# Performance work log

Measured on AMD Instinct MI355X. Metric: run time of the kernel, lower is better.

Reference implementation:

```python
import jax, jax.numpy as jnp
import numpy as np

B, S, L, D, M = 32, 256, 64, 100, 20  # batch, n_sentences, max_sentence_len, embed_dim, n_memories


def setup_inputs() -> dict:
    key = jax.random.key(0)
    ks = jax.random.split(key, 6)
    batch = jax.random.normal(ks[0], (B, S, L, D), dtype=jnp.float32)
    enc_mult = jnp.ones((L, D), dtype=jnp.float32)  # input_encoder_multiplier (init to ones)
    keys = 0.1 * jax.random.normal(ks[1], (M, D), dtype=jnp.float32)
    U = 0.1 * jax.random.normal(ks[2], (D, D), dtype=jnp.float32)  # nn.Linear weight [out,in]
    V = 0.1 * jax.random.normal(ks[3], (D, D), dtype=jnp.float32)
    W = 0.1 * jax.random.normal(ks[4], (D, D), dtype=jnp.float32)
    prelu_a = jnp.ones((), dtype=jnp.float32)  # PReLU(init=1), single shared parameter
    return {"batch": batch, "enc_mult": enc_mult, "keys": keys, "U": U, "V": V, "W": W, "prelu_a": prelu_a}


def reference(batch, enc_mult, keys, U, V, W, prelu_a):
    # Encode: elementwise multiply by learned positional multiplier, sum over words -> [B, S, D]
    enc = (batch * enc_mult).sum(axis=2)

    def prelu(x):
        return jnp.where(x >= 0, x, prelu_a * x)

    # keys @ V.T is step-invariant
    keysV = jnp.einsum('md,ed->me', keys, V)  # [M, D]

    def step(mem, s):  # mem: [B, M, D], s: [B, D]
        memory_gate = jnp.einsum('bd,bmd->bm', s, mem)          # [B, M]
        key_gate = jnp.einsum('bd,md->bm', s, keys)              # [B, M]
        gate = jax.nn.sigmoid(memory_gate + key_gate)            # [B, M]
        cand = prelu(
            jnp.einsum('bmd,ed->bme', mem, U)                    # U(memories)
            + keysV[None, :, :]                                  # V(keys)
            + jnp.einsum('bd,ed->be', s, W)[:, None, :]          # W(sentence), broadcast over M
        )
        mem = mem + cand * gate[:, :, None]
        mem = mem / jnp.linalg.norm(mem, axis=2, keepdims=True)  # L2 normalize each memory slot
        return mem, None

    mem0 = jnp.broadcast_to(keys[None, :, :], (B, M, D))  # memories init = keys repeated per batch
    mem_final, _ = jax.lax.scan(step, mem0, jnp.swapaxes(enc, 0, 1))  # scan over sentences
    return mem_final
```

## Files before the change

### kernel.cpp

```cpp
#include <hip/hip_runtime.h>


typedef float v2f __attribute__((ext_vector_type(2)));

__global__ __launch_bounds__(256) void encode_k(
    const float* __restrict__ batch,
    const float* __restrict__ encm,
    float* __restrict__ enc)
{
    const int tid = blockIdx.x * 256 + threadIdx.x;
    const int r = tid / 25;
    const int c = tid % 25;
    const float4* b4 = (const float4*)batch + (size_t)r * 1600 + c;
    const float4* e4 = (const float4*)encm + c;
    float4 a0 = {0.f,0.f,0.f,0.f}, a1 = {0.f,0.f,0.f,0.f};
    #pragma unroll 8
    for (int l = 0; l < 64; l += 2) {
        float4 x0 = b4[l * 25],       mu0 = e4[l * 25];
        float4 x1 = b4[(l + 1) * 25], mu1 = e4[(l + 1) * 25];
        a0.x += x0.x * mu0.x; a0.y += x0.y * mu0.y; a0.z += x0.z * mu0.z; a0.w += x0.w * mu0.w;
        a1.x += x1.x * mu1.x; a1.y += x1.y * mu1.y; a1.z += x1.z * mu1.z; a1.w += x1.w * mu1.w;
    }
    float4 s;
    s.x = a0.x + a1.x; s.y = a0.y + a1.y; s.z = a0.z + a1.z; s.w = a0.w + a1.w;
    ((float4*)enc)[(size_t)r * 25 + c] = s;
}

__global__ void prep_k(const float* __restrict__ W,
                       const float* __restrict__ keys,
                       float* __restrict__ T)
{
    const int d = blockIdx.x;
    const int e = threadIdx.x;
    float v = 0.f;
    if (e < 100) v = W[e * 100 + d];
    else if (e < 120) v = keys[(e - 100) * 100 + d];
    T[d * 128 + e] = v;
}

__global__ __launch_bounds__(128) void project_k(
    const float* __restrict__ enc,
    const float* __restrict__ T,
    float* __restrict__ sWp,
    float* __restrict__ kg)
{
    __shared__ float encS[400];
    const int t = threadIdx.x;
    const int row0 = blockIdx.x * 4;
    if (t < 100) ((float4*)encS)[t] = ((const float4*)(enc + (size_t)row0 * 100))[t];
    __syncthreads();
    float a0 = 0.f, a1 = 0.f, a2 = 0.f, a3 = 0.f;
    #pragma unroll 4
    for (int d = 0; d < 100; ++d) {
        const float w = T[d * 128 + t];
        a0 += w * encS[d];
        a1 += w * encS[100 + d];
        a2 += w * encS[200 + d];
        a3 += w * encS[300 + d];
    }
    if (t < 100) {
        sWp[(size_t)row0 * 100 + t]       = a0;
        sWp[(size_t)(row0 + 1) * 100 + t] = a1;
        sWp[(size_t)(row0 + 2) * 100 + t] = a2;
        sWp[(size_t)(row0 + 3) * 100 + t] = a3;
    } else if (t < 120) {
        const int m = t - 100;
        kg[(size_t)row0 * 20 + m]       = a0;
        kg[(size_t)(row0 + 1) * 20 + m] = a1;
        kg[(size_t)(row0 + 2) * 20 + m] = a2;
        kg[(size_t)(row0 + 3) * 20 + m] = a3;
    }
}

template <int CTRL>
__device__ __forceinline__ float dpp_add_f(float x) {
    int s = __builtin_amdgcn_update_dpp(0, __float_as_int(x), CTRL, 0xF, 0xF, true);
    return x + __int_as_float(s);
}
__device__ __forceinline__ float lane63(float x) {
    return __int_as_float(__builtin_amdgcn_readlane(__float_as_int(x), 63));
}

#define MATVEC100(RES, SRC4)                                                   \
    {                                                                          \
        v2f A0 = {0.f,0.f}, A1 = {0.f,0.f}, A2 = {0.f,0.f}, A3 = {0.f,0.f};    \
        _Pragma("unroll")                                                      \
        for (int k = 0; k < 25; ++k) {                                         \
            float4 v = (SRC4)[k];                                              \
            A0 += Upk[4 * k + 0] * v.x;                                        \
            A1 += Upk[4 * k + 1] * v.y;                                        \
            A2 += Upk[4 * k + 2] * v.z;                                        \
            A3 += Upk[4 * k + 3] * v.w;                                        \
        }                                                                      \
        RES = (A0 + A1) + (A2 + A3);                                           \
    }

__global__ __launch_bounds__(64, 1) void entnet_scan(
    const float* __restrict__ enc,
    const float* __restrict__ sWp,
    const float* __restrict__ kg,
    const float* __restrict__ keys,
    const float* __restrict__ U,
    const float* __restrict__ V,
    const float* __restrict__ paPtr,
    float* __restrict__ out)
{
    __shared__ float4 cand4[32];
    float* candF = (float*)cand4;
    const int lane = threadIdx.x;
    const int b = blockIdx.x / 20;
    const int m = blockIdx.x % 20;
    const bool hi = (lane < 36);
    const float h = hi ? 1.f : 0.f;
    const int e0 = lane;
    const int e1 = hi ? (64 + lane) : 99;
    const float pa = paPtr[0];

    v2f Upk[100];
    {
        const float4* u0 = (const float4*)(U + e0 * 100);
        const float4* u1 = (const float4*)(U + e1 * 100);
        #pragma unroll
        for (int k = 0; k < 25; ++k) {
            float4 a = u0[k], c = u1[k];
            Upk[4 * k + 0] = (v2f){a.x, c.x};
            Upk[4 * k + 1] = (v2f){a.y, c.y};
            Upk[4 * k + 2] = (v2f){a.z, c.z};
            Upk[4 * k + 3] = (v2f){a.w, c.w};
        }
    }
    float kv0 = 0.f, kv1 = 0.f;
    {
        const float4* km = (const float4*)(keys + m * 100);
        const float4* v0 = (const float4*)(V + e0 * 100);
        const float4* v1 = (const float4*)(V + e1 * 100);
        #pragma unroll
        for (int k = 0; k < 25; ++k) {
            float4 kk = km[k], a = v0[k], c = v1[k];
            kv0 += a.x * kk.x + a.y * kk.y + a.z * kk.z + a.w * kk.w;
            kv1 += c.x * kk.x + c.y * kk.y + c.z * kk.z + c.w * kk.w;
        }
    }
    const float k0 = keys[m * 100 + e0];
    const float k1 = h * keys[m * 100 + e1];
    float nm0 = k0, nm1 = k1;
    candF[lane] = nm0;
    candF[64 + lane] = nm1;
    __asm__ __volatile__("" ::: "memory");

    v2f P;
    MATVEC100(P, cand4);

    float nq = k0 * k0 + k1 * k1;
    nq = dpp_add_f<0x111>(nq); nq = dpp_add_f<0x112>(nq); nq = dpp_add_f<0x114>(nq);
    nq = dpp_add_f<0x118>(nq); nq = dpp_add_f<0x142>(nq); nq = dpp_add_f<0x143>(nq);
    float nsq = lane63(nq);
    float rn = 1.f;

    const float* encRow = enc + (size_t)b * 25600;
    const float* sWRow  = sWp + (size_t)b * 25600;
    const float* kgRow  = kg + (size_t)b * 5120 + m;

    float sv0 = encRow[e0], sv1 = encRow[e1];
    float sw0 = sWRow[e0],  sw1 = sWRow[e1];
    float kgc = kgRow[0];

    for (int step = 0; step < 256; ++step) {
        const int nxt = (step < 255 ? step + 1 : 255);
        const float nsv0 = encRow[nxt * 100 + e0], nsv1 = encRow[nxt * 100 + e1];
        const float nsw0 = sWRow[nxt * 100 + e0], nsw1 = sWRow[nxt * 100 + e1];
        const float nkg  = kgRow[nxt * 20];

        const float x0 = rn * P.x + kv0 + sw0;
        const float x1 = rn * P.y + kv1 + sw1;
        float c0 = (x0 >= 0.f) ? x0 : pa * x0;
        float c1 = (x1 >= 0.f) ? x1 : pa * x1;
        c1 *= h;

        candF[lane] = c0;
        candF[64 + lane] = c1;
        __asm__ __volatile__("" ::: "memory");

        float q1 = sv0 * nm0 + sv1 * nm1;
        float q3 = nm0 * c0 + nm1 * c1;
        float p4 = c0 * c0 + c1 * c1;
        #define RND3(C) q1 = dpp_add_f<C>(q1); q3 = dpp_add_f<C>(q3); p4 = dpp_add_f<C>(p4);
        RND3(0x111) RND3(0x112) RND3(0x114) RND3(0x118) RND3(0x142) RND3(0x143)
        #undef RND3

        v2f Q;
        MATVEC100(Q, cand4);

        const float Q1 = lane63(q1);
        const float Q3 = lane63(q3);
        const float P4 = lane63(p4);

        const float g = 1.f / (1.f + __expf(-(rn * Q1 + kgc)));

        nm0 = rn * nm0 + g * c0;
        nm1 = rn * nm1 + g * c1;
        P = rn * P + g * Q;

        const float n2 = nsq + 2.f * (g * rn) * Q3 + g * g * P4;
        rn = rsqrtf(n2);
        nsq = 1.f;

        sv0 = nsv0; sv1 = nsv1; sw0 = nsw0; sw1 = nsw1; kgc = nkg;
    }
    float* orow = out + (size_t)(b * 20 + m) * 100;
    orow[e0] = nm0 * rn;
    if (hi) orow[e1] = nm1 * rn;
}

extern "C" void kernel_launch(void* const* d_in, const int* in_sizes, int n_in,
                              void* d_out, int out_size, void* d_ws, size_t ws_size,
                              hipStream_t stream) {
    const float* batch = (const float*)d_in[0];
    const float* encm  = (const float*)d_in[1];
    const float* keys  = (const float*)d_in[2];
    const float* U     = (const float*)d_in[3];
    const float* V     = (const float*)d_in[4];
    const float* W     = (const float*)d_in[5];
    const float* pa    = (const float*)d_in[6];
    float* out = (float*)d_out;

    float* enc = (float*)d_ws;
    float* sWp = enc + 819200;
    float* kgb = sWp + 819200;
    float* T   = kgb + 163840;

    encode_k<<<800, 256, 0, stream>>>(batch, encm, enc);
    prep_k<<<100, 128, 0, stream>>>(W, keys, T);
    project_k<<<2048, 128, 0, stream>>>(enc, T, sWp, kgb);
    entnet_scan<<<640, 64, 0, stream>>>(enc, sWp, kgb, keys, U, V, pa, out);
}
```

Before: 529.5 us.

## Restructure encode reduction via LDS and software-pipeline gate computation in scan

```diff
diff --git a/kernel.cpp b/kernel.cpp
--- a/kernel.cpp
+++ b/kernel.cpp
@@ -3,27 +3,41 @@
 
 typedef float v2f __attribute__((ext_vector_type(2)));
 
-__global__ __launch_bounds__(256) void encode_k(
+__global__ __launch_bounds__(320) void encode_k(
     const float* __restrict__ batch,
     const float* __restrict__ encm,
     float* __restrict__ enc)
 {
-    const int tid = blockIdx.x * 256 + threadIdx.x;
-    const int r = tid / 25;
-    const int c = tid % 25;
-    const float4* b4 = (const float4*)batch + (size_t)r * 1600 + c;
-    const float4* e4 = (const float4*)encm + c;
-    float4 a0 = {0.f,0.f,0.f,0.f}, a1 = {0.f,0.f,0.f,0.f};
-    #pragma unroll 8
-    for (int l = 0; l < 64; l += 2) {
-        float4 x0 = b4[l * 25],       mu0 = e4[l * 25];
-        float4 x1 = b4[(l + 1) * 25], mu1 = e4[(l + 1) * 25];
-        a0.x += x0.x * mu0.x; a0.y += x0.y * mu0.y; a0.z += x0.z * mu0.z; a0.w += x0.w * mu0.w;
-        a1.x += x1.x * mu1.x; a1.y += x1.y * mu1.y; a1.z += x1.z * mu1.z; a1.w += x1.w * mu1.w;
-    }
-    float4 s;
-    s.x = a0.x + a1.x; s.y = a0.y + a1.y; s.z = a0.z + a1.z; s.w = a0.w + a1.w;
-    ((float4*)enc)[(size_t)r * 25 + c] = s;
+    __shared__ float prod[6400];
+    __shared__ float part[200];
+    const int t = threadIdx.x;
+    const int row = blockIdx.x;
+    const float4* rb = (const float4*)batch + (size_t)row * 1600;
+    const float4* e4 = (const float4*)encm;
+    float4* p4 = (float4*)prod;
+    #pragma unroll
+    for (int i = 0; i < 5; ++i) {
+        const int idx = i * 320 + t;
+        float4 x = rb[idx];
+        float4 mu = e4[idx];
+        float4 p;
+        p.x = x.x * mu.x; p.y = x.y * mu.y; p.z = x.z * mu.z; p.w = x.w * mu.w;
+        p4[idx] = p;
+    }
+    __syncthreads();
+    if (t < 200) {
+        const int c = (t < 100) ? t : (t - 100);
+        const int l0 = (t < 100) ? 0 : 32;
+        float s0 = 0.f, s1 = 0.f;
+        #pragma unroll
+        for (int l = 0; l < 32; l += 2) {
+            s0 += prod[(l0 + l) * 100 + c];
+            s1 += prod[(l0 + l + 1) * 100 + c];
+        }
+        part[t] = s0 + s1;
+    }
+    __syncthreads();
+    if (t < 100) enc[(size_t)row * 100 + t] = part[t] + part[100 + t];
 }
 
 __global__ void prep_k(const float* __restrict__ W,
@@ -80,6 +94,8 @@
 __device__ __forceinline__ float lane63(float x) {
     return __int_as_float(__builtin_amdgcn_readlane(__float_as_int(x), 63));
 }
+#define DPP6(v) v = dpp_add_f<0x111>(v); v = dpp_add_f<0x112>(v); v = dpp_add_f<0x114>(v); \
+                v = dpp_add_f<0x118>(v); v = dpp_add_f<0x142>(v); v = dpp_add_f<0x143>(v);
 
 #define MATVEC100(RES, SRC4)                                                   \
     {                                                                          \
@@ -95,7 +111,8 @@
         RES = (A0 + A1) + (A2 + A3);                                           \
     }
 
-__global__ __launch_bounds__(64, 1) void entnet_scan(
+__global__ __attribute__((amdgpu_waves_per_eu(1, 1))) __launch_bounds__(64)
+void entnet_scan(
     const float* __restrict__ enc,
     const float* __restrict__ sWp,
     const float* __restrict__ kg,
@@ -152,8 +169,7 @@
     MATVEC100(P, cand4);
 
     float nq = k0 * k0 + k1 * k1;
-    nq = dpp_add_f<0x111>(nq); nq = dpp_add_f<0x112>(nq); nq = dpp_add_f<0x114>(nq);
-    nq = dpp_add_f<0x118>(nq); nq = dpp_add_f<0x142>(nq); nq = dpp_add_f<0x143>(nq);
+    DPP6(nq)
     float nsq = lane63(nq);
     float rn = 1.f;
 
@@ -161,9 +177,16 @@
     const float* sWRow  = sWp + (size_t)b * 25600;
     const float* kgRow  = kg + (size_t)b * 5120 + m;
 
-    float sv0 = encRow[e0], sv1 = encRow[e1];
-    float sw0 = sWRow[e0],  sw1 = sWRow[e1];
-    float kgc = kgRow[0];
+    float sw0 = sWRow[e0], sw1 = sWRow[e1];
+    float g;
+    {
+        const float sv0 = encRow[e0], sv1 = encRow[e1];
+        const float kg0 = kgRow[0];
+        float q1 = sv0 * nm0 + sv1 * nm1;
+        DPP6(q1)
+        const float Q1 = lane63(q1);
+        g = 1.f / (1.f + __expf(-(Q1 + kg0)));
+    }
 
     for (int step = 0; step < 256; ++step) {
         const int nxt = (step < 255 ? step + 1 : 255);
@@ -176,37 +199,38 @@
         float c0 = (x0 >= 0.f) ? x0 : pa * x0;
         float c1 = (x1 >= 0.f) ? x1 : pa * x1;
         c1 *= h;
-
         candF[lane] = c0;
         candF[64 + lane] = c1;
         __asm__ __volatile__("" ::: "memory");
 
-        float q1 = sv0 * nm0 + sv1 * nm1;
         float q3 = nm0 * c0 + nm1 * c1;
         float p4 = c0 * c0 + c1 * c1;
-        #define RND3(C) q1 = dpp_add_f<C>(q1); q3 = dpp_add_f<C>(q3); p4 = dpp_add_f<C>(p4);
-        RND3(0x111) RND3(0x112) RND3(0x114) RND3(0x118) RND3(0x142) RND3(0x143)
-        #undef RND3
+        #define RND2(C) q3 = dpp_add_f<C>(q3); p4 = dpp_add_f<C>(p4);
+        RND2(0x111) RND2(0x112) RND2(0x114) RND2(0x118) RND2(0x142) RND2(0x143)
+        #undef RND2
 
         v2f Q;
         MATVEC100(Q, cand4);
 
-        const float Q1 = lane63(q1);
         const float Q3 = lane63(q3);
         const float P4 = lane63(p4);
-
-        const float g = 1.f / (1.f + __expf(-(rn * Q1 + kgc)));
+        const float n2 = nsq + 2.f * (g * rn) * Q3 + g * g * P4;
+        const float rnn = rsqrtf(n2);
+        nsq = 1.f;
 
         nm0 = rn * nm0 + g * c0;
         nm1 = rn * nm1 + g * c1;
         P = rn * P + g * Q;
 
-        const float n2 = nsq + 2.f * (g * rn) * Q3 + g * g * P4;
-        rn = rsqrtf(n2);
-        nsq = 1.f;
-
-        sv0 = nsv0; sv1 = nsv1; sw0 = nsw0; sw1 = nsw1; kgc = nkg;
-    }
+        float q1 = nsv0 * nm0 + nsv1 * nm1;
+        DPP6(q1)
+        const float Q1 = lane63(q1);
+        g = 1.f / (1.f + __expf(-(rnn * Q1 + nkg)));
+
+        rn = rnn;
+        sw0 = nsw0; sw1 = nsw1;
+    }
+    const float* dummy = V;  (void)dummy;
     float* orow = out + (size_t)(b * 20 + m) * 100;
     orow[e0] = nm0 * rn;
     if (hi) orow[e1] = nm1 * rn;
@@ -229,7 +253,7 @@
     float* kgb = sWp + 819200;
     float* T   = kgb + 163840;
 
-    encode_k<<<800, 256, 0, stream>>>(batch, encm, enc);
+    encode_k<<<8192, 320, 0, stream>>>(batch, encm, enc);
     prep_k<<<100, 128, 0, stream>>>(W, keys, T);
     project_k<<<2048, 128, 0, stream>>>(enc, T, sWp, kgb);
     entnet_scan<<<640, 64, 0, stream>>>(enc, sWp, kgb, keys, U, V, pa, out);
```

Measured after the change: 515.6 us. 1.03x faster.
